# Optimization experiments

Measured on AMD Instinct MI355X. Metric: run time of the kernel, lower is better.

Reference implementation:

```python
import jax, jax.numpy as jnp
import numpy as np

VOCAB = 32000
EMBED = 128
ENC_H = 64
DEC_H = 66


def _lstm_cell(xg, h, c, W_hh):
    # xg: [B,4H] precomputed input contribution (+bias); torch gate order i,f,g,o
    g = xg + h @ W_hh.T
    i, f, gg, o = jnp.split(g, 4, axis=-1)
    i = jax.nn.sigmoid(i)
    f = jax.nn.sigmoid(f)
    gg = jnp.tanh(gg)
    o = jax.nn.sigmoid(o)
    c = f * c + i * gg
    h = o * jnp.tanh(c)
    return h, c


def setup_inputs() -> dict:
    key = jax.random.key(0)
    ks = jax.random.split(key, 16)
    B, S, T = 128, 1024, 512
    u = lambda k, shape, scale: jax.random.uniform(k, shape, jnp.float32, -scale, scale)
    se = 1.0 / np.sqrt(ENC_H)
    sd = 1.0 / np.sqrt(DEC_H)
    sf = 1.0 / np.sqrt(DEC_H)
    return {
        "x": jax.random.randint(ks[0], (B, S), 0, VOCAB),
        "c": jax.random.normal(ks[1], (B, T, DEC_H), jnp.float32),
        "emb": jax.random.normal(ks[2], (VOCAB, EMBED), jnp.float32),
        "enc_W_ih": u(ks[3], (4 * ENC_H, EMBED), se),
        "enc_W_hh": u(ks[4], (4 * ENC_H, ENC_H), se),
        "enc_b_ih": u(ks[5], (4 * ENC_H,), se),
        "enc_b_hh": u(ks[6], (4 * ENC_H,), se),
        "dec_W_ih": u(ks[7], (4 * DEC_H, EMBED), sd),
        "dec_W_hh": u(ks[8], (4 * DEC_H, DEC_H), sd),
        "dec_b_ih": u(ks[9], (4 * DEC_H,), sd),
        "dec_b_hh": u(ks[10], (4 * DEC_H,), sd),
        "fc_W": u(ks[11], (EMBED, DEC_H), sf),
        "fc_b": u(ks[12], (EMBED,), sf),
    }


def reference(x, c, emb, enc_W_ih, enc_W_hh, enc_b_ih, enc_b_hh,
              dec_W_ih, dec_W_hh, dec_b_ih, dec_b_hh, fc_W, fc_b):
    B = x.shape[0]
    max_steps = c.shape[1]

    # ---- encoder: embedding + single-layer LSTM (final hidden state) ----
    xe = emb[x]                                      # [B,S,128]
    gates_x = jnp.einsum('bse,ge->bsg', xe, enc_W_ih) + (enc_b_ih + enc_b_hh)
    gates_x = jnp.swapaxes(gates_x, 0, 1)            # [S,B,4H]

    def enc_step(carry, gx):
        h, cc = carry
        h, cc = _lstm_cell(gx, h, cc, enc_W_hh)
        return (h, cc), None

    h0 = jnp.zeros((B, ENC_H), xe.dtype)
    (enc_h, _), _ = jax.lax.scan(enc_step, (h0, h0), gates_x)
    encoder_output = enc_h  # only used for batch size in original decoder

    x_in0 = jnp.broadcast_to(emb[0], (B, EMBED))     # embedding of zeros token
    db = dec_b_ih + dec_b_hh

    def dec_step(carry, _):
        h, cc, x_in = carry
        gx = x_in @ dec_W_ih.T + db
        h, cc = _lstm_cell(gx, h, cc, dec_W_hh)
        x_next = h @ fc_W.T + fc_b                   # final_fc feeds next input
        return (h, cc, x_next), h

    hd0 = jnp.zeros((B, DEC_H), xe.dtype)
    _, outs = jax.lax.scan(dec_step, (hd0, hd0, x_in0), None, length=max_steps)
    return jnp.swapaxes(outs, 0, 1)                  # [B, max_steps, 66]
```

## Files before the change

### kernel.cpp

```cpp
#include <hip/hip_runtime.h>

#define DH   66
#define GK   264
#define EMB  128
#define TSTEPS 512
#define REGION (TSTEPS*DH)

#define WT_SZ (256*68)
#define WE_SZ (8*68)

template<int C>
__device__ __forceinline__ float dpp_f(float v) {
    return __uint_as_float((unsigned)__builtin_amdgcn_update_dpp(
        0, (int)__float_as_uint(v), C, 0xF, 0xF, true));
}
__device__ __forceinline__ float qsum(float v) {
    v += dpp_f<0xB1>(v);
    v += dpp_f<0x4E>(v);
    return v;
}
__device__ __forceinline__ float sig_(float x) {
    return __builtin_amdgcn_rcpf(1.f + __builtin_amdgcn_exp2f(-1.442695041f * x));
}
__device__ __forceinline__ float th_(float x) {
    return fmaf(__builtin_amdgcn_rcpf(1.f + __builtin_amdgcn_exp2f(-2.885390082f * x)), 2.f, -1.f);
}

__global__ void fold_weights(const float* __restrict__ Wih,
                             const float* __restrict__ Whh,
                             const float* __restrict__ bih,
                             const float* __restrict__ bhh,
                             const float* __restrict__ fcW,
                             const float* __restrict__ fcb,
                             const float* __restrict__ emb0,
                             float* __restrict__ Wt, float* __restrict__ We,
                             float* __restrict__ bmain, float* __restrict__ bext,
                             float* __restrict__ g0p, float* __restrict__ g0e) {
    __shared__ float a[EMB];
    const int r = blockIdx.x;
    const int j = threadIdx.x;
    if (j < EMB) a[j] = Wih[r * EMB + j];
    __syncthreads();
    const int gate = r / DH;
    const int e    = r - gate * DH;
    if (j < 68) {
        float val = 0.f;
        if (j < DH) {
            float acc = Whh[r * DH + j];
            #pragma unroll 8
            for (int t = 0; t < EMB; ++t) acc = fmaf(a[t], fcW[t * DH + j], acc);
            val = acc;
        }
        if (e < 64) Wt[((e * 4 + (j & 3)) * 17 + (j >> 2)) * 4 + gate] = val;
        else        We[(((e - 64) * 4 + (j & 3)) * 17 + (j >> 2)) * 4 + gate] = val;
    } else if (j == 68) {
        float acc = bih[r] + bhh[r];
        #pragma unroll 8
        for (int t = 0; t < EMB; ++t) acc = fmaf(a[t], fcb[t], acc);
        if (e < 64) bmain[e * 4 + gate] = acc; else bext[(e - 64) * 4 + gate] = acc;
    } else if (j == 69) {
        float acc = bih[r] + bhh[r];
        #pragma unroll 8
        for (int t = 0; t < EMB; ++t) acc = fmaf(a[t], emb0[t], acc);
        if (e < 64) g0p[e * 4 + gate] = acc; else g0e[(e - 64) * 4 + gate] = acc;
    }
}

__global__ __launch_bounds__(256, 1)
void decode_seq(const float* __restrict__ Wt, const float* __restrict__ We,
                const float* __restrict__ bmain, const float* __restrict__ bext,
                const float* __restrict__ g0p, const float* __restrict__ g0e,
                float* __restrict__ hseq) {
    __shared__ __align__(16) float hT[2][4][20];
    const int tid = threadIdx.x;
    const int gt  = tid & 3;
    const int q   = tid >> 2;
    const int par = q & 1;

    const float4* wp = reinterpret_cast<const float4*>(Wt + tid * 68);
    const float4 m0 = wp[0],  m1 = wp[1],  m2 = wp[2],  m3 = wp[3];
    const float4 m4 = wp[4],  m5 = wp[5],  m6 = wp[6],  m7 = wp[7];
    const float4 m8 = wp[8],  m9 = wp[9],  m10 = wp[10], m11 = wp[11];
    const float4 m12 = wp[12], m13 = wp[13], m14 = wp[14], m15 = wp[15];
    const float4 m16 = wp[16];
    const float4* xp = reinterpret_cast<const float4*>(We + (par * 4 + gt) * 68);
    const float4 x0 = xp[0],  x1 = xp[1],  x2 = xp[2],  x3 = xp[3];
    const float4 x4 = xp[4],  x5 = xp[5],  x6 = xp[6],  x7 = xp[7];
    const float4 x8 = xp[8],  x9 = xp[9],  x10 = xp[10], x11 = xp[11];
    const float4 x12 = xp[12], x13 = xp[13], x14 = xp[14], x15 = xp[15];
    const float4 x16 = xp[16];
    const float4 bm = reinterpret_cast<const float4*>(bmain)[q];
    const float4 be = reinterpret_cast<const float4*>(bext)[par];
    float4 ga = reinterpret_cast<const float4*>(g0p)[q];
    float4 gb = reinterpret_cast<const float4*>(g0e)[par];
    float c = 0.f, c2 = 0.f;

    if (tid < 4) hT[tid & 1][2 + (tid >> 1)][16] = 0.f;

    const bool wA  = (gt == 0);
    const bool wE  = (tid == 0) | (tid == 4);
    float* hpA = hseq + q;
    float* hpE = hseq + 64 + par;

    #pragma unroll 2
    for (int step = 0; ; ++step) {
        const int b = step & 1;

        const float iv = sig_(ga.x), fv = sig_(ga.y), gv = th_(ga.z), ov = sig_(ga.w);
        c = fmaf(fv, c, iv * gv);
        const float h = ov * th_(c);
        const float i2 = sig_(gb.x), f2 = sig_(gb.y), g2 = th_(gb.z), o2 = sig_(gb.w);
        c2 = fmaf(f2, c2, i2 * g2);
        const float h2 = o2 * th_(c2);

        if (wA) { hT[b][q & 3][q >> 2] = h;  *hpA = h;  }
        if (wE) { hT[b][par][16]       = h2; *hpE = h2; }
        hpA += DH; hpE += DH;

        if (step == TSTEPS - 1) break;

        asm volatile("s_waitcnt lgkmcnt(0)\n\ts_barrier" ::: "memory");

        const float4* hr = reinterpret_cast<const float4*>(&hT[b][gt][0]);
        const float4 p0 = hr[0], p1 = hr[1], p2 = hr[2], p3 = hr[3];
        const float  px = hT[b][gt][16];

        float ai = 0.f, af = 0.f, ag = 0.f, ao = 0.f;
        float bi = 0.f, bf = 0.f, bg = 0.f, bo = 0.f;
        #define KSTEP(HK, WM, WX) \
            ai = fmaf(HK, WM.x, ai); af = fmaf(HK, WM.y, af); \
            ag = fmaf(HK, WM.z, ag); ao = fmaf(HK, WM.w, ao); \
            bi = fmaf(HK, WX.x, bi); bf = fmaf(HK, WX.y, bf); \
            bg = fmaf(HK, WX.z, bg); bo = fmaf(HK, WX.w, bo);
        KSTEP(p0.x, m0,  x0)  KSTEP(p0.y, m1,  x1)
        KSTEP(p0.z, m2,  x2)  KSTEP(p0.w, m3,  x3)
        KSTEP(p1.x, m4,  x4)  KSTEP(p1.y, m5,  x5)
        KSTEP(p1.z, m6,  x6)  KSTEP(p1.w, m7,  x7)
        KSTEP(p2.x, m8,  x8)  KSTEP(p2.y, m9,  x9)
        KSTEP(p2.z, m10, x10) KSTEP(p2.w, m11, x11)
        KSTEP(p3.x, m12, x12) KSTEP(p3.y, m13, x13)
        KSTEP(p3.z, m14, x14) KSTEP(p3.w, m15, x15)
        KSTEP(px,   m16, x16)
        #undef KSTEP

        ga = make_float4(bm.x + qsum(ai), bm.y + qsum(af),
                         bm.z + qsum(ag), bm.w + qsum(ao));
        gb = make_float4(be.x + qsum(bi), be.y + qsum(bf),
                         be.z + qsum(bg), be.w + qsum(bo));
    }
}

__global__ void bcast_out(const float4* src_base, float4* dst_base) {
    const int TILE = 1056;
    const float4* src = src_base + (blockIdx.x & 7) * TILE;
    float4* dst = dst_base + (size_t)(blockIdx.x + 8) * TILE;
    #pragma unroll 2
    for (int i = threadIdx.x; i < TILE; i += 256) dst[i] = src[i];
}

extern "C" void kernel_launch(void* const* d_in, const int* in_sizes, int n_in,
                              void* d_out, int out_size, void* d_ws, size_t ws_size,
                              hipStream_t stream) {
    const float* emb  = (const float*)d_in[2];
    const float* dWih = (const float*)d_in[7];
    const float* dWhh = (const float*)d_in[8];
    const float* dbih = (const float*)d_in[9];
    const float* dbhh = (const float*)d_in[10];
    const float* fcW  = (const float*)d_in[11];
    const float* fcb  = (const float*)d_in[12];
    float* out = (float*)d_out;

    const size_t need = (size_t)(WT_SZ + WE_SZ + 256 + 8 + 256 + 8) * sizeof(float);
    float* scratch = (ws_size >= need) ? (float*)d_ws : (out + REGION);
    float* Wt    = scratch;
    float* We    = Wt + WT_SZ;
    float* bmain = We + WE_SZ;
    float* bext  = bmain + 256;
    float* g0p   = bext + 8;
    float* g0e   = g0p + 256;

    fold_weights<<<GK, 128, 0, stream>>>(dWih, dWhh, dbih, dbhh, fcW, fcb, emb,
                                         Wt, We, bmain, bext, g0p, g0e);
    decode_seq<<<1, 256, 0, stream>>>(Wt, We, bmain, bext, g0p, g0e,
                                      out );
    bcast_out<<<127 * 8, 256, 0, stream>>>((const float4*)out, (float4*)out);
}
```

Measured before the change: 371.5 us.

## Distribute gate activations across quad lanes and shrink extra-unit FMA work

Pre-scales the folded weights and biases by log2(e) factors so each lane evaluates a single activation with one exp2 and one rcp, then broadcasts the four gate values within the quad using DPP. The two extra hidden units' dot products are split so each lane accumulates one column instead of eight, followed by a quad reduction and a ds_bpermute to scatter the gate values. The per-step reduction is changed to a transpose-style exchange so every lane ends with its own gate sum. This is meant to cut the transcendental and FMA count on the serial recurrence critical path. In exchange it adds DPP and bpermute latency on that same path.

```diff
diff --git a/kernel.cpp b/kernel.cpp
--- a/kernel.cpp
+++ b/kernel.cpp
@@ -7,7 +7,10 @@
 #define REGION (TSTEPS*DH)
 
 #define WT_SZ (256*68)
-#define WE_SZ (8*68)
+#define WEX_SZ (32*20)
+
+#define L2E  1.442695041f
+#define L2E2 2.885390082f
 
 template<int C>
 __device__ __forceinline__ float dpp_f(float v) {
@@ -19,11 +22,13 @@
     v += dpp_f<0x4E>(v);
     return v;
 }
-__device__ __forceinline__ float sig_(float x) {
-    return __builtin_amdgcn_rcpf(1.f + __builtin_amdgcn_exp2f(-1.442695041f * x));
-}
-__device__ __forceinline__ float th_(float x) {
-    return fmaf(__builtin_amdgcn_rcpf(1.f + __builtin_amdgcn_exp2f(-2.885390082f * x)), 2.f, -1.f);
+template<int K>
+__device__ __forceinline__ float quad_bc(float v) {
+    return __uint_as_float((unsigned)__builtin_amdgcn_update_dpp(
+        0, (int)__float_as_uint(v), K * 0x55, 0xF, 0xF, true));
+}
+__device__ __forceinline__ float th_c(float x) {
+    return fmaf(__builtin_amdgcn_rcpf(1.f + __builtin_amdgcn_exp2f(-L2E2 * x)), 2.f, -1.f);
 }
 
 __global__ void fold_weights(const float* __restrict__ Wih,
@@ -33,7 +38,7 @@
                              const float* __restrict__ fcW,
                              const float* __restrict__ fcb,
                              const float* __restrict__ emb0,
-                             float* __restrict__ Wt, float* __restrict__ We,
+                             float* __restrict__ Wt, float* __restrict__ Wex,
                              float* __restrict__ bmain, float* __restrict__ bext,
                              float* __restrict__ g0p, float* __restrict__ g0e) {
     __shared__ float a[EMB];
@@ -43,39 +48,47 @@
     __syncthreads();
     const int gate = r / DH;
     const int e    = r - gate * DH;
+    const float s  = (gate == 2) ? L2E2 : L2E;
     if (j < 68) {
         float val = 0.f;
         if (j < DH) {
             float acc = Whh[r * DH + j];
             #pragma unroll 8
             for (int t = 0; t < EMB; ++t) acc = fmaf(a[t], fcW[t * DH + j], acc);
-            val = acc;
+            val = acc * s;
         }
         if (e < 64) Wt[((e * 4 + (j & 3)) * 17 + (j >> 2)) * 4 + gate] = val;
-        else        We[(((e - 64) * 4 + (j & 3)) * 17 + (j >> 2)) * 4 + gate] = val;
+        else {
+            const int qq = gate * 2 + (e - 64);
+            Wex[(qq * 4 + (j & 3)) * 20 + (j >> 2)] = val;
+        }
     } else if (j == 68) {
         float acc = bih[r] + bhh[r];
         #pragma unroll 8
         for (int t = 0; t < EMB; ++t) acc = fmaf(a[t], fcb[t], acc);
+        acc *= s;
         if (e < 64) bmain[e * 4 + gate] = acc; else bext[(e - 64) * 4 + gate] = acc;
     } else if (j == 69) {
         float acc = bih[r] + bhh[r];
         #pragma unroll 8
         for (int t = 0; t < EMB; ++t) acc = fmaf(a[t], emb0[t], acc);
+        acc *= s;
         if (e < 64) g0p[e * 4 + gate] = acc; else g0e[(e - 64) * 4 + gate] = acc;
     }
 }
 
 __global__ __launch_bounds__(256, 1)
-void decode_seq(const float* __restrict__ Wt, const float* __restrict__ We,
+void decode_seq(const float* __restrict__ Wt, const float* __restrict__ Wex,
                 const float* __restrict__ bmain, const float* __restrict__ bext,
                 const float* __restrict__ g0p, const float* __restrict__ g0e,
                 float* __restrict__ hseq) {
     __shared__ __align__(16) float hT[2][4][20];
-    const int tid = threadIdx.x;
-    const int gt  = tid & 3;
-    const int q   = tid >> 2;
-    const int par = q & 1;
+    const int tid  = threadIdx.x;
+    const int lane = tid & 63;
+    const int gt   = tid & 3;
+    const int q    = tid >> 2;
+    const int parX = (lane >> 2) & 1;
+    const int qqP  = (lane >> 2) & 7;
 
     const float4* wp = reinterpret_cast<const float4*>(Wt + tid * 68);
     const float4 m0 = wp[0],  m1 = wp[1],  m2 = wp[2],  m3 = wp[3];
@@ -83,38 +96,48 @@
     const float4 m8 = wp[8],  m9 = wp[9],  m10 = wp[10], m11 = wp[11];
     const float4 m12 = wp[12], m13 = wp[13], m14 = wp[14], m15 = wp[15];
     const float4 m16 = wp[16];
-    const float4* xp = reinterpret_cast<const float4*>(We + (par * 4 + gt) * 68);
-    const float4 x0 = xp[0],  x1 = xp[1],  x2 = xp[2],  x3 = xp[3];
-    const float4 x4 = xp[4],  x5 = xp[5],  x6 = xp[6],  x7 = xp[7];
-    const float4 x8 = xp[8],  x9 = xp[9],  x10 = xp[10], x11 = xp[11];
-    const float4 x12 = xp[12], x13 = xp[13], x14 = xp[14], x15 = xp[15];
-    const float4 x16 = xp[16];
-    const float4 bm = reinterpret_cast<const float4*>(bmain)[q];
-    const float4 be = reinterpret_cast<const float4*>(bext)[par];
-    float4 ga = reinterpret_cast<const float4*>(g0p)[q];
-    float4 gb = reinterpret_cast<const float4*>(g0e)[par];
+    const float* xbase = Wex + (qqP * 4 + gt) * 20;
+    const float4 xv0 = reinterpret_cast<const float4*>(xbase)[0];
+    const float4 xv1 = reinterpret_cast<const float4*>(xbase)[1];
+    const float4 xv2 = reinterpret_cast<const float4*>(xbase)[2];
+    const float4 xv3 = reinterpret_cast<const float4*>(xbase)[3];
+    const float  xv4 = xbase[16];
+
+    const float bsel = bmain[tid];
+    const float bx   = bext[(qqP & 1) * 4 + (qqP >> 1)];
+    float g   = g0p[tid];
+    float gbx = g0e[parX * 4 + gt];
     float c = 0.f, c2 = 0.f;
 
+    const float m1c = (gt == 2) ? 2.f : 1.f;
+    const float m0c = (gt == 2) ? -1.f : 0.f;
+    const int bpaddr = (((gt << 1) | parX) << 2) << 2;
+
     if (tid < 4) hT[tid & 1][2 + (tid >> 1)][16] = 0.f;
 
-    const bool wA  = (gt == 0);
-    const bool wE  = (tid == 0) | (tid == 4);
+    const bool wA = (gt == 0);
+    const bool wE = (tid == 0) | (tid == 4);
     float* hpA = hseq + q;
-    float* hpE = hseq + 64 + par;
+    float* hpE = hseq + 64 + parX;
 
     #pragma unroll 2
     for (int step = 0; ; ++step) {
         const int b = step & 1;
 
-        const float iv = sig_(ga.x), fv = sig_(ga.y), gv = th_(ga.z), ov = sig_(ga.w);
+        const float v  = fmaf(__builtin_amdgcn_rcpf(1.f + __builtin_amdgcn_exp2f(-g)), m1c, m0c);
+        const float iv = quad_bc<0>(v), fv = quad_bc<1>(v);
+        const float gv = quad_bc<2>(v), ov = quad_bc<3>(v);
         c = fmaf(fv, c, iv * gv);
-        const float h = ov * th_(c);
-        const float i2 = sig_(gb.x), f2 = sig_(gb.y), g2 = th_(gb.z), o2 = sig_(gb.w);
-        c2 = fmaf(f2, c2, i2 * g2);
-        const float h2 = o2 * th_(c2);
+        const float h = ov * th_c(c);
+
+        const float vx  = fmaf(__builtin_amdgcn_rcpf(1.f + __builtin_amdgcn_exp2f(-gbx)), m1c, m0c);
+        const float iv2 = quad_bc<0>(vx), fv2 = quad_bc<1>(vx);
+        const float gv2 = quad_bc<2>(vx), ov2 = quad_bc<3>(vx);
+        c2 = fmaf(fv2, c2, iv2 * gv2);
+        const float h2 = ov2 * th_c(c2);
 
         if (wA) { hT[b][q & 3][q >> 2] = h;  *hpA = h;  }
-        if (wE) { hT[b][par][16]       = h2; *hpE = h2; }
+        if (wE) { hT[b][parX][16]      = h2; *hpE = h2; }
         hpA += DH; hpE += DH;
 
         if (step == TSTEPS - 1) break;
@@ -125,28 +148,33 @@
         const float4 p0 = hr[0], p1 = hr[1], p2 = hr[2], p3 = hr[3];
         const float  px = hT[b][gt][16];
 
-        float ai = 0.f, af = 0.f, ag = 0.f, ao = 0.f;
-        float bi = 0.f, bf = 0.f, bg = 0.f, bo = 0.f;
+        float ai = 0.f, af = 0.f, ag = 0.f, ao = 0.f, ax = 0.f;
         #define KSTEP(HK, WM, WX) \
             ai = fmaf(HK, WM.x, ai); af = fmaf(HK, WM.y, af); \
             ag = fmaf(HK, WM.z, ag); ao = fmaf(HK, WM.w, ao); \
-            bi = fmaf(HK, WX.x, bi); bf = fmaf(HK, WX.y, bf); \
-            bg = fmaf(HK, WX.z, bg); bo = fmaf(HK, WX.w, bo);
-        KSTEP(p0.x, m0,  x0)  KSTEP(p0.y, m1,  x1)
-        KSTEP(p0.z, m2,  x2)  KSTEP(p0.w, m3,  x3)
-        KSTEP(p1.x, m4,  x4)  KSTEP(p1.y, m5,  x5)
-        KSTEP(p1.z, m6,  x6)  KSTEP(p1.w, m7,  x7)
-        KSTEP(p2.x, m8,  x8)  KSTEP(p2.y, m9,  x9)
-        KSTEP(p2.z, m10, x10) KSTEP(p2.w, m11, x11)
-        KSTEP(p3.x, m12, x12) KSTEP(p3.y, m13, x13)
-        KSTEP(p3.z, m14, x14) KSTEP(p3.w, m15, x15)
-        KSTEP(px,   m16, x16)
+            ax = fmaf(HK, WX, ax);
+        KSTEP(p0.x, m0,  xv0.x)  KSTEP(p0.y, m1,  xv0.y)
+        KSTEP(p0.z, m2,  xv0.z)  KSTEP(p0.w, m3,  xv0.w)
+        KSTEP(p1.x, m4,  xv1.x)  KSTEP(p1.y, m5,  xv1.y)
+        KSTEP(p1.z, m6,  xv1.z)  KSTEP(p1.w, m7,  xv1.w)
+        KSTEP(p2.x, m8,  xv2.x)  KSTEP(p2.y, m9,  xv2.y)
+        KSTEP(p2.z, m10, xv2.z)  KSTEP(p2.w, m11, xv2.w)
+        KSTEP(p3.x, m12, xv3.x)  KSTEP(p3.y, m13, xv3.y)
+        KSTEP(p3.z, m14, xv3.z)  KSTEP(p3.w, m15, xv3.w)
+        KSTEP(px,   m16, xv4)
         #undef KSTEP
 
-        ga = make_float4(bm.x + qsum(ai), bm.y + qsum(af),
-                         bm.z + qsum(ag), bm.w + qsum(ao));
-        gb = make_float4(be.x + qsum(bi), be.y + qsum(bf),
-                         be.z + qsum(bg), be.w + qsum(bo));
+        const bool s1 = (gt & 1), s2h = (gt & 2);
+        float keepA = s1 ? af : ai, sendA = s1 ? ai : af;
+        float keepB = s1 ? ao : ag, sendB = s1 ? ag : ao;
+        const float x1 = keepA + dpp_f<0xB1>(sendA);
+        const float x2 = keepB + dpp_f<0xB1>(sendB);
+        float keep2 = s2h ? x2 : x1, send2 = s2h ? x1 : x2;
+        g = bsel + keep2 + dpp_f<0x4E>(send2);
+
+        const float sx = qsum(ax) + bx;
+        gbx = __uint_as_float((unsigned)__builtin_amdgcn_ds_bpermute(
+            bpaddr, (int)__float_as_uint(sx)));
     }
 }
 
@@ -170,18 +198,18 @@
     const float* fcb  = (const float*)d_in[12];
     float* out = (float*)d_out;
 
-    const size_t need = (size_t)(WT_SZ + WE_SZ + 256 + 8 + 256 + 8) * sizeof(float);
+    const size_t need = (size_t)(WT_SZ + WEX_SZ + 256 + 8 + 256 + 8) * sizeof(float);
     float* scratch = (ws_size >= need) ? (float*)d_ws : (out + REGION);
     float* Wt    = scratch;
-    float* We    = Wt + WT_SZ;
-    float* bmain = We + WE_SZ;
+    float* Wex   = Wt + WT_SZ;
+    float* bmain = Wex + WEX_SZ;
     float* bext  = bmain + 256;
     float* g0p   = bext + 8;
     float* g0e   = g0p + 256;
 
     fold_weights<<<GK, 128, 0, stream>>>(dWih, dWhh, dbih, dbhh, fcW, fcb, emb,
-                                         Wt, We, bmain, bext, g0p, g0e);
-    decode_seq<<<1, 256, 0, stream>>>(Wt, We, bmain, bext, g0p, g0e,
+                                         Wt, Wex, bmain, bext, g0p, g0e);
+    decode_seq<<<1, 256, 0, stream>>>(Wt, Wex, bmain, bext, g0p, g0e,
                                       out );
     bcast_out<<<127 * 8, 256, 0, stream>>>((const float4*)out, (float4*)out);
 }
```

Measured after the change: 318.3 us. -14.3%, faster.
